# Kernel tuning notes

Measured on AMD Instinct MI355X. Metric: run time of the kernel, lower is better.

Reference implementation:

```python
import jax, jax.numpy as jnp
import numpy as np

HEADS = 16
HEAD_DIM = 64
EMBED = HEADS * HEAD_DIM  # 1024
N, L = 4, 4096


def setup_inputs() -> dict:
    key = jax.random.key(0)
    k1, k2, k3, k4, k5, k6, k7, k8 = jax.random.split(key, 8)
    s = 0.02
    return {
        "q": jax.random.normal(k1, (N, L, EMBED), jnp.float32),
        "k": jax.random.normal(k2, (N, L, EMBED), jnp.float32),
        "v": jax.random.normal(k3, (N, L, EMBED), jnp.float32),
        "mask": jnp.ones((N, L, HEADS, HEADS), jnp.int32),
        # torch Linear weights: (out_features, in_features)
        "q_w": jax.random.normal(k4, (HEAD_DIM, HEAD_DIM), jnp.float32) * s,
        "k_w": jax.random.normal(k5, (HEAD_DIM, HEAD_DIM), jnp.float32) * s,
        "v_w": jax.random.normal(k6, (HEAD_DIM, HEAD_DIM), jnp.float32) * s,
        "fc_w": jax.random.normal(k7, (EMBED, EMBED), jnp.float32) * s,
        "fc_b": jax.random.normal(k8, (EMBED,), jnp.float32) * s,
    }


def reference(q, k, v, mask, q_w, k_w, v_w, fc_w, fc_b):
    n, ql = q.shape[0], q.shape[1]
    # reshape to (N, L, H, D) and apply per-head-dim linear projections (x @ W.T)
    q4 = q.reshape(n, ql, HEADS, HEAD_DIM) @ q_w.T
    k4 = k.reshape(n, k.shape[1], HEADS, HEAD_DIM) @ k_w.T
    v4 = v.reshape(n, v.shape[1], HEADS, HEAD_DIM) @ v_w.T
    # Faithful to the original: matmul broadcasts over (N, L), contracting head_dim,
    # so logits are (N, L, H, H) -- attention across heads per token.
    scale = 1.0 / jnp.sqrt(jnp.float32(HEAD_DIM))
    logits = jnp.einsum("nlhd,nlgd->nlhg", q4, k4) * scale
    logits = jnp.where(mask == 0, -jnp.inf, logits)
    weights = jax.nn.softmax(logits, axis=-1)
    out4 = jnp.einsum("nlhg,nlgd->nlhd", weights, v4)  # (N, L, H, D)
    # Faithful scrambled reshape: permute to (N, H, L, D) then flatten to (N, L, H*D)
    out = out4.transpose(0, 2, 1, 3).reshape(n, ql, HEADS * HEAD_DIM)
    return out @ fc_w.T + fc_b
```

## Files before the change

### kernel.cpp

```cpp
#include <hip/hip_runtime.h>
#include <hip/hip_bf16.h>
#include <stdint.h>

#define TOKENS 16384
#define LSEQ 4096
#define WPAD 72

typedef short bf16x8 __attribute__((ext_vector_type(8)));
typedef float f32x4 __attribute__((ext_vector_type(4)));

typedef __attribute__((address_space(1))) void as1_t;
typedef __attribute__((address_space(3))) void as3_t;

__device__ __forceinline__ unsigned short f2bf(float x) {
  __hip_bfloat16 t = __float2bfloat16(x);
  return *reinterpret_cast<unsigned short*>(&t);
}

__device__ __forceinline__ bf16x8 pack8(float4 a, float4 b) {
  bf16x8 t;
  t[0] = (short)f2bf(a.x); t[1] = (short)f2bf(a.y);
  t[2] = (short)f2bf(a.z); t[3] = (short)f2bf(a.w);
  t[4] = (short)f2bf(b.x); t[5] = (short)f2bf(b.y);
  t[6] = (short)f2bf(b.z); t[7] = (short)f2bf(b.w);
  return t;
}

__device__ __forceinline__ void async16(const void* g, void* lds) {
  __builtin_amdgcn_global_load_lds((as1_t*)const_cast<void*>(g),
                                   (as3_t*)lds, 16, 0, 0);
}

__global__ __launch_bounds__(256) void cvt_prep(
    const float* __restrict__ fcw, unsigned short* __restrict__ Wb,
    const float* __restrict__ qw, const float* __restrict__ kw,
    const float* __restrict__ vw, unsigned short* __restrict__ Mout,
    unsigned short* __restrict__ vwout) {
  const int b = blockIdx.x, t = threadIdx.x;
  if (b < 1024) {
    const int i = b * 256 + t;
    float4 f = ((const float4*)fcw)[i];
    union { unsigned short us[4]; uint2 u2; } pk;
    pk.us[0] = f2bf(f.x); pk.us[1] = f2bf(f.y);
    pk.us[2] = f2bf(f.z); pk.us[3] = f2bf(f.w);
    ((uint2*)Wb)[i] = pk.u2;
    return;
  }
  __shared__ float ql[4096], kl[4096];
#pragma unroll
  for (int j = 0; j < 4; ++j) {
    const int i = t + j * 256;
    ((float4*)ql)[i] = ((const float4*)qw)[i];
    ((float4*)kl)[i] = ((const float4*)kw)[i];
    float4 f = ((const float4*)vw)[i];
    union { unsigned short us[4]; uint2 u2; } pk;
    pk.us[0] = f2bf(f.x); pk.us[1] = f2bf(f.y);
    pk.us[2] = f2bf(f.z); pk.us[3] = f2bf(f.w);
    ((uint2*)vwout)[i] = pk.u2;
  }
  __syncthreads();
  const int f = t >> 2;
  const int e0 = (t & 3) * 16;
  float4 a0 = {}, a1 = {}, a2 = {}, a3 = {};
#pragma unroll 8
  for (int d = 0; d < 64; ++d) {
    const float qv = ql[d * 64 + f];
    const float* kr = &kl[d * 64 + e0];
    const float4 k0 = *(const float4*)(kr);
    const float4 k1 = *(const float4*)(kr + 4);
    const float4 k2 = *(const float4*)(kr + 8);
    const float4 k3 = *(const float4*)(kr + 12);
    a0.x += qv * k0.x; a0.y += qv * k0.y; a0.z += qv * k0.z; a0.w += qv * k0.w;
    a1.x += qv * k1.x; a1.y += qv * k1.y; a1.z += qv * k1.z; a1.w += qv * k1.w;
    a2.x += qv * k2.x; a2.y += qv * k2.y; a2.z += qv * k2.z; a2.w += qv * k2.w;
    a3.x += qv * k3.x; a3.y += qv * k3.y; a3.z += qv * k3.z; a3.w += qv * k3.w;
  }
  union { unsigned short us[8]; uint4 u4; } p0, p1;
  p0.us[0] = f2bf(a0.x); p0.us[1] = f2bf(a0.y); p0.us[2] = f2bf(a0.z); p0.us[3] = f2bf(a0.w);
  p0.us[4] = f2bf(a1.x); p0.us[5] = f2bf(a1.y); p0.us[6] = f2bf(a1.z); p0.us[7] = f2bf(a1.w);
  p1.us[0] = f2bf(a2.x); p1.us[1] = f2bf(a2.y); p1.us[2] = f2bf(a2.z); p1.us[3] = f2bf(a2.w);
  p1.us[4] = f2bf(a3.x); p1.us[5] = f2bf(a3.y); p1.us[6] = f2bf(a3.z); p1.us[7] = f2bf(a3.w);
  *(uint4*)&Mout[f * 64 + e0] = p0.u4;
  *(uint4*)&Mout[f * 64 + e0 + 8] = p1.u4;
}

__global__ __launch_bounds__(256, 6) void attn11(
    const float* __restrict__ q, const float* __restrict__ k,
    const float* __restrict__ v, const int* __restrict__ mask,
    const unsigned short* __restrict__ Mg, const unsigned short* __restrict__ vwg,
    unsigned short* __restrict__ X) {
  __shared__ unsigned short Ml[64 * WPAD];
  __shared__ unsigned short Vw[64 * WPAD];
  __shared__ unsigned short scr[4][16 * WPAD];

  const int tid = threadIdx.x;
  const int l = tid & 63, w = tid >> 6;
  const int lr = l & 15, lg = l >> 4;

  const int tok = blockIdx.x * 4 + w;
  const size_t tb = (size_t)tok * 1024;
  const int off = lr * 64 + lg * 8;

  const float4 qa = *(const float4*)(q + tb + off);
  const float4 qb = *(const float4*)(q + tb + off + 4);
  const float4 qc = *(const float4*)(q + tb + off + 32);
  const float4 qd = *(const float4*)(q + tb + off + 36);
  const float4 ka = *(const float4*)(k + tb + off);
  const float4 kb = *(const float4*)(k + tb + off + 4);
  const float4 kc = *(const float4*)(k + tb + off + 32);
  const float4 kd = *(const float4*)(k + tb + off + 36);
  const float4 va = *(const float4*)(v + tb + off);
  const float4 vb = *(const float4*)(v + tb + off + 4);
  const float4 vc = *(const float4*)(v + tb + off + 32);
  const float4 vd = *(const float4*)(v + tb + off + 36);
  const int4 mk4 = *(const int4*)(mask + (size_t)tok * 256 + lr * 16 + lg * 4);

  {
    const int row = tid >> 2, c0 = (tid & 3) * 16;
    *(uint4*)&Ml[row * WPAD + c0]     = *(const uint4*)(Mg + row * 64 + c0);
    *(uint4*)&Ml[row * WPAD + c0 + 8] = *(const uint4*)(Mg + row * 64 + c0 + 8);
    *(uint4*)&Vw[row * WPAD + c0]     = *(const uint4*)(vwg + row * 64 + c0);
    *(uint4*)&Vw[row * WPAD + c0 + 8] = *(const uint4*)(vwg + row * 64 + c0 + 8);
  }
  __syncthreads();

  const bf16x8 ak0 = pack8(ka, kb), ak1 = pack8(kc, kd);
  const bf16x8 av0 = pack8(va, vb), av1 = pack8(vc, vd);
  const bf16x8 aq0 = pack8(qa, qb), aq1 = pack8(qc, qd);

  f32x4 accu[4], accv[4];
#pragma unroll
  for (int n = 0; n < 4; ++n) {
    const int wrow = (n * 16 + lr) * WPAD;
    f32x4 z = {};
    const bf16x8 bm0 = *(const bf16x8*)&Ml[wrow + lg * 8];
    const bf16x8 bm1 = *(const bf16x8*)&Ml[wrow + 32 + lg * 8];
    accu[n] = __builtin_amdgcn_mfma_f32_16x16x32_bf16(ak0, bm0, z, 0, 0, 0);
    accu[n] = __builtin_amdgcn_mfma_f32_16x16x32_bf16(ak1, bm1, accu[n], 0, 0, 0);
    const bf16x8 bw0 = *(const bf16x8*)&Vw[wrow + lg * 8];
    const bf16x8 bw1 = *(const bf16x8*)&Vw[wrow + 32 + lg * 8];
    accv[n] = __builtin_amdgcn_mfma_f32_16x16x32_bf16(av0, bw0, z, 0, 0, 0);
    accv[n] = __builtin_amdgcn_mfma_f32_16x16x32_bf16(av1, bw1, accv[n], 0, 0, 0);
  }

  unsigned short* U = scr[w];
#pragma unroll
  for (int n = 0; n < 4; ++n)
#pragma unroll
    for (int r = 0; r < 4; ++r)
      U[(lg * 4 + r) * WPAD + n * 16 + lr] = f2bf(accu[n][r]);

  const bf16x8 ua0 = *(const bf16x8*)&U[lr * WPAD + lg * 8];
  const bf16x8 ua1 = *(const bf16x8*)&U[lr * WPAD + 32 + lg * 8];
  f32x4 z4 = {};
  f32x4 st = __builtin_amdgcn_mfma_f32_16x16x32_bf16(ua0, aq0, z4, 0, 0, 0);
  st = __builtin_amdgcn_mfma_f32_16x16x32_bf16(ua1, aq1, st, 0, 0, 0);

  float e[4];
  float sm = 0.f;
  const int mks[4] = {mk4.x, mk4.y, mk4.z, mk4.w};
#pragma unroll
  for (int r = 0; r < 4; ++r) {
    e[r] = (mks[r] != 0) ? __expf(st[r] * 0.125f) : 0.f;
    sm += e[r];
  }
  sm += __shfl_xor(sm, 16);
  sm += __shfl_xor(sm, 32);
  const float inv = 1.0f / sm;
#pragma unroll
  for (int r = 0; r < 4; ++r) e[r] *= inv;

  bf16x8 apv;
#pragma unroll
  for (int j = 0; j < 8; ++j) {
    const int srcg = (lg * 2 + (j >> 2)) & 3;
    const float pv = __shfl(e[j & 3], lr + srcg * 16, 64);
    apv[j] = (short)((lg < 2) ? f2bf(pv) : (unsigned short)0);
  }

  const int s0 = lr + ((lg & 1) * 2) * 16;
  const int s1 = s0 + 16;
  f32x4 o[4];
#pragma unroll
  for (int n = 0; n < 4; ++n) {
    bf16x8 bv;
#pragma unroll
    for (int j = 0; j < 8; ++j) {
      const float xv = __shfl(accv[n][j & 3], (j < 4) ? s0 : s1, 64);
      bv[j] = (short)f2bf(xv);
    }
    f32x4 z = {};
    o[n] = __builtin_amdgcn_mfma_f32_16x16x32_bf16(apv, bv, z, 0, 0, 0);
  }

#pragma unroll
  for (int n = 0; n < 4; ++n)
#pragma unroll
    for (int r = 0; r < 4; ++r)
      U[(lg * 4 + r) * WPAD + n * 16 + lr] = f2bf(o[n][r]);

  const int nb = tok >> 12, lpos = tok & (LSEQ - 1);
#pragma unroll
  for (int it = 0; it < 2; ++it) {
    const int idx = it * 64 + l;
    const int h = idx >> 3, c = idx & 7;
    const uint4 val = *(const uint4*)&U[h * WPAD + c * 8];
    *(uint4*)&X[((size_t)(nb * 16 + h) * LSEQ + lpos) * 64 + c * 8] = val;
  }
}

__global__ __launch_bounds__(256) void gemm_fc(const unsigned short* __restrict__ A,
                                               const unsigned short* __restrict__ B,
                                               const float* __restrict__ bias,
                                               float* __restrict__ C) {
  __shared__ unsigned short sA[128 * 32];
  __shared__ unsigned short sB[128 * 32];
  const int tid = threadIdx.x;
  const int l = tid & 63, w = tid >> 6;
  const int wr = w >> 1, wc = w & 1;

  const int bid = blockIdx.x;
  const int wg = (bid & 7) * 128 + (bid >> 3);
  const int tm = (wg >> 3) * 128;
  const int tn = (wg & 7) * 128;

  f32x4 acc[4][4] = {};

  const int r0 = w * 16 + (l >> 2);
  const int c8 = (l & 3) * 8;

  for (int kt = 0; kt < 32; ++kt) {
    const int k0 = kt * 32;
#pragma unroll
    for (int s = 0; s < 2; ++s) {
      async16(A + (size_t)(tm + s * 64 + r0) * 1024 + k0 + c8,
              (char*)sA + s * 4096 + w * 1024);
      async16(B + (size_t)(tn + s * 64 + r0) * 1024 + k0 + c8,
              (char*)sB + s * 4096 + w * 1024);
    }
    __syncthreads();

    bf16x8 af[4], bfr[4];
#pragma unroll
    for (int fi = 0; fi < 4; ++fi)
      af[fi] = *(const bf16x8*)((const char*)sA +
                                (wr * 64 + fi * 16 + (l & 15)) * 64 + (l >> 4) * 16);
#pragma unroll
    for (int fj = 0; fj < 4; ++fj)
      bfr[fj] = *(const bf16x8*)((const char*)sB +
                                 (wc * 64 + fj * 16 + (l & 15)) * 64 + (l >> 4) * 16);
#pragma unroll
    for (int fi = 0; fi < 4; ++fi)
#pragma unroll
      for (int fj = 0; fj < 4; ++fj)
        acc[fi][fj] = __builtin_amdgcn_mfma_f32_16x16x32_bf16(af[fi], bfr[fj],
                                                              acc[fi][fj], 0, 0, 0);
    __syncthreads();
  }

#pragma unroll
  for (int fj = 0; fj < 4; ++fj) {
    const int col = tn + wc * 64 + fj * 16 + (l & 15);
    const float bv = bias[col];
#pragma unroll
    for (int fi = 0; fi < 4; ++fi) {
#pragma unroll
      for (int r = 0; r < 4; ++r) {
        const int row = tm + wr * 64 + fi * 16 + (l >> 4) * 4 + r;
        C[(size_t)row * 1024 + col] = acc[fi][fj][r] + bv;
      }
    }
  }
}

extern "C" void kernel_launch(void* const* d_in, const int* in_sizes, int n_in,
                              void* d_out, int out_size, void* d_ws, size_t ws_size,
                              hipStream_t stream) {
  (void)in_sizes; (void)n_in; (void)out_size; (void)ws_size;
  const float* q   = (const float*)d_in[0];
  const float* k   = (const float*)d_in[1];
  const float* v   = (const float*)d_in[2];
  const int*  mask = (const int*)d_in[3];
  const float* qw  = (const float*)d_in[4];
  const float* kw  = (const float*)d_in[5];
  const float* vw  = (const float*)d_in[6];
  const float* fcw = (const float*)d_in[7];
  const float* fcb = (const float*)d_in[8];
  float* out = (float*)d_out;

  unsigned short* X   = (unsigned short*)d_ws;
  unsigned short* Wb  = X + (size_t)16 * 1024 * 1024;
  unsigned short* Mw  = Wb + (size_t)1024 * 1024;
  unsigned short* vwb = Mw + 4096;

  cvt_prep<<<dim3(1025), dim3(256), 0, stream>>>(fcw, Wb, qw, kw, vw, Mw, vwb);
  attn11<<<dim3(4096), dim3(256), 0, stream>>>(q, k, v, mask, Mw, vwb, X);
  gemm_fc<<<dim3(1024), dim3(256), 0, stream>>>(X, Wb, fcb, out);
}
```

Measured before the change: 109.9 us.

## Replace FC GEMM with 256x256-tile, 8-wave, double-buffered LDS pipeline

Rewrites the final fc GEMM to use 256x256 output tiles with 512 threads and a 128 KB LDS double buffer. Asynchronous global-to-LDS loads for the next K-step are interleaved with MFMA phases, and XOR-swizzled LDS addressing is used to cut bank conflicts. The aim is to raise arithmetic intensity and hide load latency behind compute. In exchange the kernel runs at one block per CU with heavy register use, and only 256 blocks are launched, which may underfill the device.

After: 102.3 us (median of 2 runs). 1.07x faster.

```diff
diff --git a/kernel.cpp b/kernel.cpp
--- a/kernel.cpp
+++ b/kernel.cpp
@@ -30,6 +30,7 @@
   __builtin_amdgcn_global_load_lds((as1_t*)const_cast<void*>(g),
                                    (as3_t*)lds, 16, 0, 0);
 }
+#define WAITCNT(n) asm volatile("s_waitcnt vmcnt(" #n ")" ::: "memory")
 
 __global__ __launch_bounds__(256) void cvt_prep(
     const float* __restrict__ fcw, unsigned short* __restrict__ Wb,
@@ -209,67 +210,143 @@
   }
 }
 
-__global__ __launch_bounds__(256) void gemm_fc(const unsigned short* __restrict__ A,
-                                               const unsigned short* __restrict__ B,
-                                               const float* __restrict__ bias,
-                                               float* __restrict__ C) {
-  __shared__ unsigned short sA[128 * 32];
-  __shared__ unsigned short sB[128 * 32];
+__global__ __launch_bounds__(512, 1) void gemm_fc8(
+    const unsigned short* __restrict__ A,
+    const unsigned short* __restrict__ B,
+    const float* __restrict__ bias,
+    float* __restrict__ C) {
+  __shared__ char lds[131072];
+
   const int tid = threadIdx.x;
-  const int l = tid & 63, w = tid >> 6;
-  const int wr = w >> 1, wc = w & 1;
+  const int l = tid & 63;
+  const int wv = tid >> 6;
+  const int wr = wv >> 2;
+  const int wc = wv & 3;
+  const int lr = l & 15, lg = l >> 4;
 
   const int bid = blockIdx.x;
-  const int wg = (bid & 7) * 128 + (bid >> 3);
-  const int tm = (wg >> 3) * 128;
-  const int tn = (wg & 7) * 128;
-
-  f32x4 acc[4][4] = {};
-
-  const int r0 = w * 16 + (l >> 2);
-  const int c8 = (l & 3) * 8;
-
-  for (int kt = 0; kt < 32; ++kt) {
-    const int k0 = kt * 32;
-#pragma unroll
-    for (int s = 0; s < 2; ++s) {
-      async16(A + (size_t)(tm + s * 64 + r0) * 1024 + k0 + c8,
-              (char*)sA + s * 4096 + w * 1024);
-      async16(B + (size_t)(tn + s * 64 + r0) * 1024 + k0 + c8,
-              (char*)sB + s * 4096 + w * 1024);
+  const int wg = (bid & 7) * 32 + (bid >> 3);
+  const int tm = (wg >> 2) * 256;
+  const int tn = (wg & 3) * 256;
+
+  const int srow = wv * 8 + (l >> 3);
+  const int schunk = (l & 7) ^ (2 * ((l >> 5) & 1));
+
+  auto stage_unit = [&](int u) {
+    const int kt = u >> 2, t = u & 3, h = t & 1;
+    const unsigned short* src =
+        (t < 2) ? (A + (size_t)(tm + h * 128) * 1024)
+                : (B + (size_t)(tn + h * 128) * 1024);
+    const int k0 = kt * 64;
+    char* dst = lds + (u & 7) * 16384 + wv * 1024;
+#pragma unroll
+    for (int li = 0; li < 2; ++li) {
+      const int r = li * 64 + srow;
+      async16(src + (size_t)r * 1024 + k0 + schunk * 8, dst + li * 8192);
     }
-    __syncthreads();
-
-    bf16x8 af[4], bfr[4];
-#pragma unroll
-    for (int fi = 0; fi < 4; ++fi)
-      af[fi] = *(const bf16x8*)((const char*)sA +
-                                (wr * 64 + fi * 16 + (l & 15)) * 64 + (l >> 4) * 16);
+  };
+
+#pragma unroll
+  for (int u = 0; u < 4; ++u) stage_unit(u);
+  WAITCNT(0);
+  __builtin_amdgcn_s_barrier();
+
+  f32x4 acc[8][4] = {};
+  const int swz = ((lr >> 2) & 1) * 32;
+  const int arow0 = lr * 128;
+  const int brow0 = ((wc & 1) * 64 + lr) * 128;
+
+#pragma unroll 1
+  for (int j = 0; j < 16; ++j) {
+    const char* abase = lds + ((j & 1) * 4 + wr) * 16384;
+    const char* bbase = lds + ((j & 1) * 4 + 2 + (wc >> 1)) * 16384;
+    bf16x8 bfr[4], af[4];
+
 #pragma unroll
     for (int fj = 0; fj < 4; ++fj)
-      bfr[fj] = *(const bf16x8*)((const char*)sB +
-                                 (wc * 64 + fj * 16 + (l & 15)) * 64 + (l >> 4) * 16);
-#pragma unroll
-    for (int fi = 0; fi < 4; ++fi)
+      bfr[fj] = *(const bf16x8*)(bbase + brow0 + fj * 2048 + ((lg * 16) ^ swz));
+#pragma unroll
+    for (int mi = 0; mi < 4; ++mi)
+      af[mi] = *(const bf16x8*)(abase + arow0 + mi * 2048 + ((lg * 16) ^ swz));
+    if (j < 15) stage_unit(4 * j + 4);
+    __builtin_amdgcn_sched_barrier(0);
+    __builtin_amdgcn_s_barrier();
+    __builtin_amdgcn_s_setprio(1);
+#pragma unroll
+    for (int mi = 0; mi < 4; ++mi)
 #pragma unroll
       for (int fj = 0; fj < 4; ++fj)
-        acc[fi][fj] = __builtin_amdgcn_mfma_f32_16x16x32_bf16(af[fi], bfr[fj],
-                                                              acc[fi][fj], 0, 0, 0);
-    __syncthreads();
+        acc[mi][fj] = __builtin_amdgcn_mfma_f32_16x16x32_bf16(af[mi], bfr[fj],
+                                                              acc[mi][fj], 0, 0, 0);
+    __builtin_amdgcn_s_setprio(0);
+    __builtin_amdgcn_s_barrier();
+
+#pragma unroll
+    for (int mi = 0; mi < 4; ++mi)
+      af[mi] = *(const bf16x8*)(abase + arow0 + 8192 + mi * 2048 + ((lg * 16) ^ swz));
+    if (j < 15) stage_unit(4 * j + 5);
+    __builtin_amdgcn_sched_barrier(0);
+    __builtin_amdgcn_s_barrier();
+    __builtin_amdgcn_s_setprio(1);
+#pragma unroll
+    for (int mi = 0; mi < 4; ++mi)
+#pragma unroll
+      for (int fj = 0; fj < 4; ++fj)
+        acc[4 + mi][fj] = __builtin_amdgcn_mfma_f32_16x16x32_bf16(af[mi], bfr[fj],
+                                                                  acc[4 + mi][fj], 0, 0, 0);
+    __builtin_amdgcn_s_setprio(0);
+    __builtin_amdgcn_s_barrier();
+
+#pragma unroll
+    for (int fj = 0; fj < 4; ++fj)
+      bfr[fj] = *(const bf16x8*)(bbase + brow0 + fj * 2048 + ((64 + lg * 16) ^ swz));
+#pragma unroll
+    for (int mi = 0; mi < 4; ++mi)
+      af[mi] = *(const bf16x8*)(abase + arow0 + mi * 2048 + ((64 + lg * 16) ^ swz));
+    if (j < 15) stage_unit(4 * j + 6);
+    __builtin_amdgcn_sched_barrier(0);
+    __builtin_amdgcn_s_barrier();
+    __builtin_amdgcn_s_setprio(1);
+#pragma unroll
+    for (int mi = 0; mi < 4; ++mi)
+#pragma unroll
+      for (int fj = 0; fj < 4; ++fj)
+        acc[mi][fj] = __builtin_amdgcn_mfma_f32_16x16x32_bf16(af[mi], bfr[fj],
+                                                              acc[mi][fj], 0, 0, 0);
+    __builtin_amdgcn_s_setprio(0);
+    __builtin_amdgcn_s_barrier();
+
+#pragma unroll
+    for (int mi = 0; mi < 4; ++mi)
+      af[mi] = *(const bf16x8*)(abase + arow0 + 8192 + mi * 2048 + ((64 + lg * 16) ^ swz));
+    if (j < 15) stage_unit(4 * j + 7);
+    __builtin_amdgcn_sched_barrier(0);
+    __builtin_amdgcn_s_barrier();
+    __builtin_amdgcn_s_setprio(1);
+#pragma unroll
+    for (int mi = 0; mi < 4; ++mi)
+#pragma unroll
+      for (int fj = 0; fj < 4; ++fj)
+        acc[4 + mi][fj] = __builtin_amdgcn_mfma_f32_16x16x32_bf16(af[mi], bfr[fj],
+                                                                  acc[4 + mi][fj], 0, 0, 0);
+    __builtin_amdgcn_s_setprio(0);
+    if (j < 15) {
+      WAITCNT(0);
+      __builtin_amdgcn_s_barrier();
+    }
   }
 
 #pragma unroll
   for (int fj = 0; fj < 4; ++fj) {
-    const int col = tn + wc * 64 + fj * 16 + (l & 15);
+    const int col = tn + wc * 64 + fj * 16 + lr;
     const float bv = bias[col];
 #pragma unroll
-    for (int fi = 0; fi < 4; ++fi) {
-#pragma unroll
-      for (int r = 0; r < 4; ++r) {
-        const int row = tm + wr * 64 + fi * 16 + (l >> 4) * 4 + r;
-        C[(size_t)row * 1024 + col] = acc[fi][fj][r] + bv;
+    for (int mf = 0; mf < 8; ++mf)
+#pragma unroll
+      for (int rr = 0; rr < 4; ++rr) {
+        const int row = tm + wr * 128 + mf * 16 + lg * 4 + rr;
+        C[(size_t)row * 1024 + col] = acc[mf][fj][rr] + bv;
       }
-    }
   }
 }
 
@@ -295,5 +372,5 @@
 
   cvt_prep<<<dim3(1025), dim3(256), 0, stream>>>(fcw, Wb, qw, kw, vw, Mw, vwb);
   attn11<<<dim3(4096), dim3(256), 0, stream>>>(q, k, v, mask, Mw, vwb, X);
-  gemm_fc<<<dim3(1024), dim3(256), 0, stream>>>(X, Wb, fcb, out);
-}
+  gemm_fc8<<<dim3(256), dim3(512), 0, stream>>>(X, Wb, fcb, out);
+}
```
